# Performance work log

Measured on AMD Instinct MI355X. Metric: run time of the kernel, lower is better.

Reference implementation:

```python
import jax, jax.numpy as jnp
import numpy as np

N, D, K = 10000, 784, 16          # nodes, input feat dim, num_neighbors
E = N * (K - 1)                   # edges
H = 128                           # hidden width in all MLPs
SIZES = [784, 128, 2]             # node_sizes


def setup_inputs() -> dict:
    key = jax.random.key(0)
    ks = jax.random.split(key, 24)
    w = lambda k, shape: jax.random.normal(k, shape, jnp.float32) * 0.02
    inp = {
        "x": jax.random.normal(ks[0], (N, D), jnp.float32),
        "edge_attr": jax.random.uniform(ks[1], (E, 1), jnp.float32),
        "idxs": jax.random.randint(ks[2], (N, K - 1), 0, N, dtype=jnp.int32),
    }
    # Layer 1: in=784, msg_size=784, out=128
    inp["l1_msg_w1"] = w(ks[3], (D + 1, H));      inp["l1_msg_b1"] = jnp.zeros((H,), jnp.float32)
    inp["l1_msg_w2"] = w(ks[4], (H, D));          inp["l1_msg_b2"] = jnp.zeros((D,), jnp.float32)
    inp["l1_node_w1"] = w(ks[5], (D + D, H));     inp["l1_node_b1"] = jnp.zeros((H,), jnp.float32)
    inp["l1_node_w2"] = w(ks[6], (H, 128));       inp["l1_node_b2"] = jnp.zeros((128,), jnp.float32)
    # Layer 2: in=128, msg_size=128, out=2
    inp["l2_msg_w1"] = w(ks[7], (128 + 1, H));    inp["l2_msg_b1"] = jnp.zeros((H,), jnp.float32)
    inp["l2_msg_w2"] = w(ks[8], (H, 128));        inp["l2_msg_b2"] = jnp.zeros((128,), jnp.float32)
    inp["l2_node_w1"] = w(ks[9], (128 + 128, H)); inp["l2_node_b1"] = jnp.zeros((H,), jnp.float32)
    inp["l2_node_w2"] = w(ks[10], (H, 2));        inp["l2_node_b2"] = jnp.zeros((2,), jnp.float32)
    return inp


def _mlp(x, w1, b1, w2, b2):
    return jax.nn.relu(x @ w1 + b1) @ w2 + b2


def _node_layer(x, src, edge_attr,
                mw1, mb1, mw2, mb2, nw1, nb1, nw2, nb2):
    # message over edges: cat(x[src], edge_attr) -> MLP   [E, msg_size]
    msg = _mlp(jnp.concatenate([x[src], edge_attr], axis=1), mw1, mb1, mw2, mb2)
    # scatter_mean by src index (faithful to the original, which uses index=src)
    sums = jax.ops.segment_sum(msg, src, num_segments=N)
    cnt = jax.ops.segment_sum(jnp.ones((src.shape[0], 1), msg.dtype), src, num_segments=N)
    agg = jnp.where(cnt > 0, sums / jnp.maximum(cnt, 1.0), 0.0)
    # node update: cat(x, agg_msg) -> MLP
    return _mlp(jnp.concatenate([x, agg], axis=1), nw1, nb1, nw2, nb2)


def reference(x, edge_attr, idxs,
              l1_msg_w1, l1_msg_b1, l1_msg_w2, l1_msg_b2,
              l1_node_w1, l1_node_b1, l1_node_w2, l1_node_b2,
              l2_msg_w1, l2_msg_b1, l2_msg_w2, l2_msg_b2,
              l2_node_w1, l2_node_b1, l2_node_w2, l2_node_b2):
    src = idxs.reshape(-1)  # [E]; dst is unused by the original message computation
    h = _node_layer(x, src, edge_attr,
                    l1_msg_w1, l1_msg_b1, l1_msg_w2, l1_msg_b2,
                    l1_node_w1, l1_node_b1, l1_node_w2, l1_node_b2)
    proj = _node_layer(h, src, edge_attr,
                       l2_msg_w1, l2_msg_b1, l2_msg_w2, l2_msg_b2,
                       l2_node_w1, l2_node_b1, l2_node_w2, l2_node_b2)  # [N, 2]
    # vectorized per-neighbor squared distances (replaces the nested python loop)
    neigh = proj[idxs]                                   # [N, K-1, 2]
    d = jnp.sum((proj[:, None, :] - neigh) ** 2, axis=-1)  # [N, K-1]
    return d.reshape(-1, 1)                              # [N*(K-1), 1]
```

## Files before the change

### kernel.cpp

```cpp
#include <hip/hip_runtime.h>

#define N_NODES 10000
#define E_EDGES 150000
#define KNB     15
#define FILL_BLOCKS 587
#define GEMM_BLOCKS 628

__global__ void count_kernel(const int* __restrict__ idxs, int* __restrict__ cnt, int e) {
    int i = blockIdx.x * blockDim.x + threadIdx.x;
    if (i < e) atomicAdd(&cnt[idxs[i]], 1);
}

__device__ __forceinline__
void gemm_tile2(const float* __restrict__ A, int K,
                const float* __restrict__ Blo, const float* __restrict__ Bhi, int ldB,
                float* __restrict__ C, int ldC, int M,
                int rowBlk, int colBlk) {
    __shared__ float As2[16][34];
    __shared__ float Bs2[16][64];
    int tid = threadIdx.x;
    int tn  = tid & 15, tm = tid >> 4;
    int arow = tid >> 3, acB = (tid & 7) << 1;
    int brow = tid >> 4, bcol = (tid & 15) << 2;
    int rowBase = rowBlk * 32, colBase = colBlk * 64;

    bool half = (Bhi != nullptr) && (colBase >= 128);
    const float* B = half ? Bhi : Blo;
    int bj = colBase - (half ? 128 : 0) + bcol;

    float2 av; float4 bv;
    auto loadA = [&](int k0, float2& dst) {
        int gr = rowBase + arow;
        if (gr < M) dst = *(const float2*)(A + (size_t)gr * K + k0 + acB);
        else { dst.x = dst.y = 0.f; }
    };
    auto loadB = [&](int k0, float4& dst) {
        dst = *(const float4*)(B + (size_t)(k0 + brow) * ldB + bj);
    };
    loadA(0, av); loadB(0, bv);

    float acc[2][4] = {};
    for (int k0 = 0; k0 < K; k0 += 16) {
        __syncthreads();
        As2[acB + 0][arow] = av.x; As2[acB + 1][arow] = av.y;
        *(float4*)&Bs2[brow][bcol] = bv;
        __syncthreads();
        if (k0 + 16 < K) { loadA(k0 + 16, av); loadB(k0 + 16, bv); }
#pragma unroll
        for (int k = 0; k < 16; ++k) {
            float4 b = *(const float4*)&Bs2[k][tn << 2];
            float2 a = *(const float2*)&As2[k][tm << 1];
            acc[0][0] = fmaf(a.x, b.x, acc[0][0]); acc[0][1] = fmaf(a.x, b.y, acc[0][1]);
            acc[0][2] = fmaf(a.x, b.z, acc[0][2]); acc[0][3] = fmaf(a.x, b.w, acc[0][3]);
            acc[1][0] = fmaf(a.y, b.x, acc[1][0]); acc[1][1] = fmaf(a.y, b.y, acc[1][1]);
            acc[1][2] = fmaf(a.y, b.z, acc[1][2]); acc[1][3] = fmaf(a.y, b.w, acc[1][3]);
        }
    }
#pragma unroll
    for (int i = 0; i < 2; ++i) {
        int row = rowBase + tm * 2 + i;
        if (row >= M) continue;
#pragma unroll
        for (int j = 0; j < 4; ++j)
            C[(size_t)row * ldC + colBase + (tn << 2) + j] = acc[i][j];
    }
}

__global__ __launch_bounds__(256)
void scanfold_kernel(const float* __restrict__ mw2, const float* __restrict__ mb2,
                     const float* __restrict__ nw1, const float* __restrict__ nb2,
                     const float* __restrict__ nw2,
                     const float* __restrict__ m2w1, const float* __restrict__ m2b1,
                     const float* __restrict__ m2w2, const float* __restrict__ m2b2,
                     const float* __restrict__ n2w1, const float* __restrict__ n2b1,
                     float* __restrict__ M1, float* __restrict__ M2,
                     float* __restrict__ WH,
                     float* __restrict__ v1, float* __restrict__ v2,
                     float* __restrict__ bu2, float* __restrict__ bx2,
                     const int* __restrict__ cnt, int* __restrict__ eoff,
                     float* __restrict__ maskv, int* __restrict__ fillc) {
    int b = blockIdx.x;
    if (b == 0) {
        __shared__ int ssum[256];
        int tid = threadIdx.x;
        const int CH = 40;
        int base = tid * CH;
        int v[CH]; int s = 0;
#pragma unroll
        for (int q = 0; q < CH; ++q) {
            int i = base + q;
            v[q] = (i < N_NODES) ? cnt[i] : 0;
            s += v[q];
        }
        ssum[tid] = s;
        __syncthreads();
        for (int off = 1; off < 256; off <<= 1) {
            int t = (tid >= off) ? ssum[tid - off] : 0;
            __syncthreads();
            ssum[tid] += t;
            __syncthreads();
        }
        int ex = ssum[tid] - s;
#pragma unroll
        for (int q = 0; q < CH; ++q) {
            int i = base + q;
            if (i < N_NODES) {
                eoff[i]  = ex;
                maskv[i] = (v[q] > 0) ? 1.f : 0.f;
                fillc[i] = 0;
                ex += v[q];
            }
        }
        return;
    }
    b -= 1;
    if (b < 8) {
        gemm_tile2(mw2, 784, nw1 + 784 * 128, nullptr, 128, M1, 128, 128, b >> 1, b & 1);
    } else if (b < 16) {
        int t = b - 8;
        gemm_tile2(m2w2, 128, n2w1 + 128 * 128, nullptr, 128, M2, 128, 128, t >> 1, t & 1);
    } else if (b < 32) {
        int t = b - 16;
        gemm_tile2(nw2, 128, m2w1, n2w1, 128, WH, 256, 128, t >> 2, t & 3);
    } else {
        __shared__ float red[256];
        int t  = (b - 32) >> 1;
        int j  = ((b - 32) & 1) * 64 + (threadIdx.x & 63);
        int kq = threadIdx.x >> 6;
        const float* bvec; const float* Bv; const float* add; float* out; int Kv;
        if (t == 0)      { bvec = mb2;  Bv = nw1 + 784 * 128;  add = nullptr; out = v1;  Kv = 784; }
        else if (t == 1) { bvec = m2b2; Bv = n2w1 + 128 * 128; add = nullptr; out = v2;  Kv = 128; }
        else if (t == 2) { bvec = nb2;  Bv = m2w1;             add = m2b1;    out = bu2; Kv = 128; }
        else             { bvec = nb2;  Bv = n2w1;             add = n2b1;    out = bx2; Kv = 128; }
        float acc = 0.f;
        for (int k = kq; k < Kv; k += 4) acc = fmaf(bvec[k], Bv[k * 128 + j], acc);
        red[threadIdx.x] = acc;
        __syncthreads();
        if (threadIdx.x < 64) {
            float tot = red[threadIdx.x] + red[threadIdx.x + 64] +
                        red[threadIdx.x + 128] + red[threadIdx.x + 192];
            out[j] = tot + (add ? add[j] : 0.f);
        }
    }
}

__device__ __forceinline__
void gemm784_tile(const float* __restrict__ A,
                  const float* __restrict__ B0, const float* __restrict__ B1,
                  const float* __restrict__ biasLo, const float* __restrict__ biasHi,
                  const float* __restrict__ vhi, const float* __restrict__ rowmask,
                  float* __restrict__ C, int M, int gb) {
    __shared__ float As[16][68];
    __shared__ float Bs[16][64];
    int rb = gb >> 2, cb = gb & 3;
    int tid = threadIdx.x;
    int tm = tid >> 4, tn = tid & 15;
    int arow = tid >> 2, ac4 = (tid & 3) << 2;
    int brow = tid >> 4, bc4 = (tid & 15) << 2;
    int rowBase = rb * 64, colBase = cb * 64;
    bool hi = colBase >= 128;
    const float* B    = hi ? B1 : B0;
    const float* bias = hi ? biasHi : biasLo;
    int bj = ((cb & 1) << 6) + bc4;

    int gr = rowBase + arow; if (gr > M - 1) gr = M - 1;
    const float* Ap = A + (size_t)gr * 784;

    float4 av, bv;
    av = *(const float4*)(Ap + ac4);
    bv = *(const float4*)(B + (size_t)brow * 128 + bj);

    float acc[4][4] = {};
    for (int k0 = 0; k0 < 784; k0 += 16) {
        __syncthreads();
        As[ac4 + 0][arow] = av.x;
        As[ac4 + 1][arow] = av.y;
        As[ac4 + 2][arow] = av.z;
        As[ac4 + 3][arow] = av.w;
        *(float4*)&Bs[brow][bc4] = bv;
        __syncthreads();
        if (k0 + 16 < 784) {
            av = *(const float4*)(Ap + k0 + 16 + ac4);
            bv = *(const float4*)(B + (size_t)(k0 + 16 + brow) * 128 + bj);
        }
#pragma unroll
        for (int k = 0; k < 16; ++k) {
            float4 a = *(const float4*)&As[k][tm << 2];
            float4 b = *(const float4*)&Bs[k][tn << 2];
            acc[0][0] = fmaf(a.x, b.x, acc[0][0]); acc[0][1] = fmaf(a.x, b.y, acc[0][1]);
            acc[0][2] = fmaf(a.x, b.z, acc[0][2]); acc[0][3] = fmaf(a.x, b.w, acc[0][3]);
            acc[1][0] = fmaf(a.y, b.x, acc[1][0]); acc[1][1] = fmaf(a.y, b.y, acc[1][1]);
            acc[1][2] = fmaf(a.y, b.z, acc[1][2]); acc[1][3] = fmaf(a.y, b.w, acc[1][3]);
            acc[2][0] = fmaf(a.z, b.x, acc[2][0]); acc[2][1] = fmaf(a.z, b.y, acc[2][1]);
            acc[2][2] = fmaf(a.z, b.z, acc[2][2]); acc[2][3] = fmaf(a.z, b.w, acc[2][3]);
            acc[3][0] = fmaf(a.w, b.x, acc[3][0]); acc[3][1] = fmaf(a.w, b.y, acc[3][1]);
            acc[3][2] = fmaf(a.w, b.z, acc[3][2]); acc[3][3] = fmaf(a.w, b.w, acc[3][3]);
        }
    }

#pragma unroll
    for (int i = 0; i < 4; ++i) {
        int row = rowBase + (tm << 2) + i;
        if (row >= M) continue;
        float rm = hi ? rowmask[row] : 0.f;
#pragma unroll
        for (int j = 0; j < 4; ++j) {
            int gcol = colBase + (tn << 2) + j;
            int cj   = gcol & 127;
            float v = acc[i][j] + bias[cj];
            if (hi) v = fmaf(rm, vhi[cj], v);
            C[(size_t)row * 256 + gcol] = v;
        }
    }
}

__global__ __launch_bounds__(256)
void fillgemm_kernel(const int* __restrict__ idxs, const float* __restrict__ ea,
                     const int* __restrict__ eoff, int* __restrict__ fillc,
                     float* __restrict__ eas,
                     const float* __restrict__ A,
                     const float* __restrict__ B0, const float* __restrict__ B1,
                     const float* __restrict__ biasLo, const float* __restrict__ biasHi,
                     const float* __restrict__ vhi, const float* __restrict__ rowmask,
                     float* __restrict__ C, int M) {
    int gb = blockIdx.x;
    if (gb < FILL_BLOCKS) {
        int i = gb * 256 + threadIdx.x;
        if (i < E_EDGES) {
            int s = idxs[i];
            int p = atomicAdd(&fillc[s], 1);
            eas[eoff[s] + p] = ea[i];
        }
        return;
    }
    gemm784_tile(A, B0, B1, biasLo, biasHi, vhi, rowmask, C, M, gb - FILL_BLOCKS);
}

__global__ __launch_bounds__(256)
void fused_mid_kernel(const float* __restrict__ UX, const float* __restrict__ wlast,
                      const float* __restrict__ eas, const int* __restrict__ eoff,
                      const int* __restrict__ cnt,
                      const float* __restrict__ Mmat, const float* __restrict__ WH,
                      const float* __restrict__ bu2, const float* __restrict__ bx2,
                      const float* __restrict__ v2,
                      float* __restrict__ UX2, int M) {
    __shared__ float mhT[128][36];
    __shared__ float ts[32][132];
    __shared__ float Bs[16][264];
    __shared__ float ebuf[1536];
    __shared__ float rmask[32];
    int rowBase = blockIdx.x * 32;
    int tid = threadIdx.x;

    {
        int d = tid & 127, sub = tid >> 7;
        float w = wlast[d];
        float uu[16], sum[16];
        int es[16], ec[16];
#pragma unroll
        for (int it = 0; it < 16; ++it) {
            int n  = rowBase + it * 2 + sub;
            int nc = (n < M) ? n : M - 1;
            ec[it] = cnt[nc];
            es[it] = eoff[nc];
            uu[it] = UX[(size_t)nc * 256 + d];
            sum[it] = 0.f;
            if (d == 0) rmask[it * 2 + sub] = (ec[it] > 0) ? 1.f : 0.f;
        }
        int ebase = eoff[rowBase];
        int eend  = (rowBase + 32 < M) ? eoff[rowBase + 32] : E_EDGES;
        for (int w0 = ebase; w0 < eend; w0 += 1536) {
            int wlen = min(1536, eend - w0);
            __syncthreads();
            for (int q = tid; q < wlen; q += 256) ebuf[q] = eas[w0 + q];
            __syncthreads();
#pragma unroll
            for (int it = 0; it < 16; ++it) {
                int lo = max(es[it], w0), hi = min(es[it] + ec[it], w0 + wlen);
                for (int e = lo; e < hi; ++e)
                    sum[it] += fmaxf(fmaf(ebuf[e - w0], w, uu[it]), 0.f);
            }
        }
#pragma unroll
        for (int it = 0; it < 16; ++it)
            mhT[d][it * 2 + sub] = (ec[it] > 0) ? sum[it] / (float)ec[it] : 0.f;
    }
    __syncthreads();

    {
        int tm = tid >> 5, tn = tid & 31;
        float acc[4][4] = {};
        for (int k0 = 0; k0 < 128; k0 += 16) {
#pragma unroll
            for (int t2 = 0; t2 < 2; ++t2) {
                int f2 = (tid << 1) | t2;
                int kr = f2 >> 5, c4 = (f2 & 31) << 2;
                *(float4*)&Bs[kr][c4] = *(const float4*)(Mmat + (size_t)(k0 + kr) * 128 + c4);
            }
            __syncthreads();
#pragma unroll
            for (int k = 0; k < 16; ++k) {
                float4 a = *(const float4*)&mhT[k0 + k][tm << 2];
                float4 b = *(const float4*)&Bs[k][tn << 2];
                acc[0][0] = fmaf(a.x, b.x, acc[0][0]); acc[0][1] = fmaf(a.x, b.y, acc[0][1]);
                acc[0][2] = fmaf(a.x, b.z, acc[0][2]); acc[0][3] = fmaf(a.x, b.w, acc[0][3]);
                acc[1][0] = fmaf(a.y, b.x, acc[1][0]); acc[1][1] = fmaf(a.y, b.y, acc[1][1]);
                acc[1][2] = fmaf(a.y, b.z, acc[1][2]); acc[1][3] = fmaf(a.y, b.w, acc[1][3]);
                acc[2][0] = fmaf(a.z, b.x, acc[2][0]); acc[2][1] = fmaf(a.z, b.y, acc[2][1]);
                acc[2][2] = fmaf(a.z, b.z, acc[2][2]); acc[2][3] = fmaf(a.z, b.w, acc[2][3]);
                acc[3][0] = fmaf(a.w, b.x, acc[3][0]); acc[3][1] = fmaf(a.w, b.y, acc[3][1]);
                acc[3][2] = fmaf(a.w, b.z, acc[3][2]); acc[3][3] = fmaf(a.w, b.w, acc[3][3]);
            }
            __syncthreads();
        }
#pragma unroll
        for (int i = 0; i < 4; ++i) {
            int row = rowBase + (tm << 2) + i;
            int rc  = (row < M) ? row : M - 1;
#pragma unroll
            for (int j = 0; j < 4; ++j) {
                int col = (tn << 2) + j;
                float v = acc[i][j] + UX[(size_t)rc * 256 + 128 + col];
                ts[(tm << 2) + i][col] = fmaxf(v, 0.f);
            }
        }
    }

    {
        int tm = tid >> 5, tn = tid & 31;
        float acc[4][8] = {};
        for (int k0 = 0; k0 < 128; k0 += 16) {
#pragma unroll
            for (int q = 0; q < 4; ++q) {
                int slot = (q << 8) + tid;
                int kr = slot >> 6, c4 = (slot & 63) << 2;
                *(float4*)&Bs[kr][c4] = *(const float4*)(WH + (size_t)(k0 + kr) * 256 + c4);
            }
            __syncthreads();
#pragma unroll
            for (int k = 0; k < 16; ++k) {
                float4 b0 = *(const float4*)&Bs[k][tn << 3];
                float4 b1 = *(const float4*)&Bs[k][(tn << 3) + 4];
                float br[8] = {b0.x, b0.y, b0.z, b0.w, b1.x, b1.y, b1.z, b1.w};
#pragma unroll
                for (int i = 0; i < 4; ++i) {
                    float a = ts[(tm << 2) + i][k0 + k];
#pragma unroll
                    for (int j = 0; j < 8; ++j)
                        acc[i][j] = fmaf(a, br[j], acc[i][j]);
                }
            }
            __syncthreads();
        }
        bool half = (tn >= 16);
        const float* bias = half ? bx2 : bu2;
#pragma unroll
        for (int i = 0; i < 4; ++i) {
            int row = rowBase + (tm << 2) + i;
            if (row >= M) continue;
            float rm = rmask[(tm << 2) + i];
            float4 o0, o1;
            float* po0 = (float*)&o0; float* po1 = (float*)&o1;
#pragma unroll
            for (int j = 0; j < 4; ++j) {
                int gcol0 = (tn << 3) + j, gcol1 = (tn << 3) + 4 + j;
                int cj0 = gcol0 & 127, cj1 = gcol1 & 127;
                float v0 = acc[i][j] + bias[cj0];
                float v1s = acc[i][4 + j] + bias[cj1];
                if (half) { v0 = fmaf(rm, v2[cj0], v0); v1s = fmaf(rm, v2[cj1], v1s); }
                po0[j] = v0; po1[j] = v1s;
            }
            float* orow = UX2 + (size_t)row * 256 + (tn << 3);
            *(float4*)(orow)     = o0;
            *(float4*)(orow + 4) = o1;
        }
    }
}

__global__ __launch_bounds__(256)
void fused_last_kernel(const float* __restrict__ UX2, const float* __restrict__ wlast,
                       const float* __restrict__ eas, const int* __restrict__ eoff,
                       const int* __restrict__ cnt,
                       const float* __restrict__ Mmat,
                       const float* __restrict__ w2, const float* __restrict__ b2,
                       float* __restrict__ proj, int M) {
    __shared__ float mhT[128][36];
    __shared__ float Bs[16][132];
    __shared__ float ebuf[1536];
    int rowBase = blockIdx.x * 32;
    int tid = threadIdx.x;

    {
        int d = tid & 127, sub = tid >> 7;
        float w = wlast[d];
        float uu[16], sum[16];
        int es[16], ec[16];
#pragma unroll
        for (int it = 0; it < 16; ++it) {
            int n  = rowBase + it * 2 + sub;
            int nc = (n < M) ? n : M - 1;
            ec[it] = cnt[nc];
            es[it] = eoff[nc];
            uu[it] = UX2[(size_t)nc * 256 + d];
            sum[it] = 0.f;
        }
        int ebase = eoff[rowBase];
        int eend  = (rowBase + 32 < M) ? eoff[rowBase + 32] : E_EDGES;
        for (int w0 = ebase; w0 < eend; w0 += 1536) {
            int wlen = min(1536, eend - w0);
            __syncthreads();
            for (int q = tid; q < wlen; q += 256) ebuf[q] = eas[w0 + q];
            __syncthreads();
#pragma unroll
            for (int it = 0; it < 16; ++it) {
                int lo = max(es[it], w0), hi = min(es[it] + ec[it], w0 + wlen);
                for (int e = lo; e < hi; ++e)
                    sum[it] += fmaxf(fmaf(ebuf[e - w0], w, uu[it]), 0.f);
            }
        }
#pragma unroll
        for (int it = 0; it < 16; ++it)
            mhT[d][it * 2 + sub] = (ec[it] > 0) ? sum[it] / (float)ec[it] : 0.f;
    }
    __syncthreads();

    int tm = tid >> 5, tn = tid & 31;
    float acc[4][4] = {};
    for (int k0 = 0; k0 < 128; k0 += 16) {
#pragma unroll
        for (int t2 = 0; t2 < 2; ++t2) {
            int f2 = (tid << 1) | t2;
            int kr = f2 >> 5, c4 = (f2 & 31) << 2;
            *(float4*)&Bs[kr][c4] = *(const float4*)(Mmat + (size_t)(k0 + kr) * 128 + c4);
        }
        __syncthreads();
#pragma unroll
        for (int k = 0; k < 16; ++k) {
            float4 a = *(const float4*)&mhT[k0 + k][tm << 2];
            float4 b = *(const float4*)&Bs[k][tn << 2];
            acc[0][0] = fmaf(a.x, b.x, acc[0][0]); acc[0][1] = fmaf(a.x, b.y, acc[0][1]);
            acc[0][2] = fmaf(a.x, b.z, acc[0][2]); acc[0][3] = fmaf(a.x, b.w, acc[0][3]);
            acc[1][0] = fmaf(a.y, b.x, acc[1][0]); acc[1][1] = fmaf(a.y, b.y, acc[1][1]);
            acc[1][2] = fmaf(a.y, b.z, acc[1][2]); acc[1][3] = fmaf(a.y, b.w, acc[1][3]);
            acc[2][0] = fmaf(a.z, b.x, acc[2][0]); acc[2][1] = fmaf(a.z, b.y, acc[2][1]);
            acc[2][2] = fmaf(a.z, b.z, acc[2][2]); acc[2][3] = fmaf(a.z, b.w, acc[2][3]);
            acc[3][0] = fmaf(a.w, b.x, acc[3][0]); acc[3][1] = fmaf(a.w, b.y, acc[3][1]);
            acc[3][2] = fmaf(a.w, b.z, acc[3][2]); acc[3][3] = fmaf(a.w, b.w, acc[3][3]);
        }
        __syncthreads();
    }

    float p0[4] = {}, p1[4] = {};
#pragma unroll
    for (int i = 0; i < 4; ++i) {
        int row = rowBase + (tm << 2) + i;
        int rc  = (row < M) ? row : M - 1;
#pragma unroll
        for (int j = 0; j < 4; ++j) {
            int col = (tn << 2) + j;
            float t = fmaxf(acc[i][j] + UX2[(size_t)rc * 256 + 128 + col], 0.f);
            p0[i] = fmaf(t, w2[col * 2],     p0[i]);
            p1[i] = fmaf(t, w2[col * 2 + 1], p1[i]);
        }
    }
#pragma unroll
    for (int i = 0; i < 4; ++i) {
        for (int off = 16; off > 0; off >>= 1) {
            p0[i] += __shfl_xor(p0[i], off, 64);
            p1[i] += __shfl_xor(p1[i], off, 64);
        }
    }
    if (tn == 0) {
#pragma unroll
        for (int i = 0; i < 4; ++i) {
            int row = rowBase + (tm << 2) + i;
            if (row < M) {
                proj[row * 2]     = p0[i] + b2[0];
                proj[row * 2 + 1] = p1[i] + b2[1];
            }
        }
    }
}

__global__ void dist_kernel(const float* __restrict__ proj, const int* __restrict__ idxs,
                            float* __restrict__ out, int e) {
    int i = blockIdx.x * blockDim.x + threadIdx.x;
    if (i >= e) return;
    int n = i / KNB;
    int m = idxs[i];
    float2 pn = *(const float2*)(proj + 2 * n);
    float2 pm = *(const float2*)(proj + 2 * m);
    float dx = pn.x - pm.x;
    float dy = pn.y - pm.y;
    out[i] = dx * dx + dy * dy;
}

extern "C" void kernel_launch(void* const* d_in, const int* in_sizes, int n_in,
                              void* d_out, int out_size, void* d_ws, size_t ws_size,
                              hipStream_t stream) {
    (void)in_sizes; (void)n_in; (void)out_size; (void)ws_size;
    const float* x    = (const float*)d_in[0];
    const float* eatt = (const float*)d_in[1];
    const int*   idxs = (const int*)d_in[2];
    const float* mw1  = (const float*)d_in[3];
    const float* mb1  = (const float*)d_in[4];
    const float* mw2  = (const float*)d_in[5];
    const float* mb2  = (const float*)d_in[6];
    const float* nw1  = (const float*)d_in[7];
    const float* nb1  = (const float*)d_in[8];
    const float* nw2  = (const float*)d_in[9];
    const float* nb2  = (const float*)d_in[10];
    const float* m2w1 = (const float*)d_in[11];
    const float* m2b1 = (const float*)d_in[12];
    const float* m2w2 = (const float*)d_in[13];
    const float* m2b2 = (const float*)d_in[14];
    const float* n2w1 = (const float*)d_in[15];
    const float* n2b1 = (const float*)d_in[16];
    const float* n2w2 = (const float*)d_in[17];
    const float* n2b2 = (const float*)d_in[18];
    float* out = (float*)d_out;

    float* fws   = (float*)d_ws;
    float* UX1   = fws;
    float* UX2   = fws + 2560000;
    float* proj  = fws + 5120000;
    float* maskv = fws + 5140000;
    float* eas   = fws + 5150016;
    float* M1    = fws + 5300016;
    float* M2    = fws + 5316400;
    float* WH    = fws + 5332784;
    float* v1    = fws + 5365552;
    float* v2    = fws + 5365680;
    float* bu2   = fws + 5365808;
    float* bx2   = fws + 5365936;
    int*   cnt   = (int*)(fws + 5366064);
    int*   fillc = cnt + N_NODES;
    int*   eoff  = fillc + N_NODES;

    hipMemsetAsync(cnt, 0, N_NODES * sizeof(int), stream);
    count_kernel<<<FILL_BLOCKS, 256, 0, stream>>>(idxs, cnt, E_EDGES);

    scanfold_kernel<<<41, 256, 0, stream>>>(mw2, mb2, nw1, nb2, nw2,
                                            m2w1, m2b1, m2w2, m2b2, n2w1, n2b1,
                                            M1, M2, WH, v1, v2, bu2, bx2,
                                            cnt, eoff, maskv, fillc);

    fillgemm_kernel<<<FILL_BLOCKS + GEMM_BLOCKS, 256, 0, stream>>>(
        idxs, eatt, eoff, fillc, eas,
        x, mw1, nw1, mb1, nb1, v1, maskv, UX1, N_NODES);

    fused_mid_kernel<<<313, 256, 0, stream>>>(UX1, mw1 + 784 * 128, eas, eoff, cnt,
                                              M1, WH, bu2, bx2, v2, UX2, N_NODES);

    fused_last_kernel<<<313, 256, 0, stream>>>(UX2, m2w1 + 128 * 128, eas, eoff, cnt,
                                               M2, n2w2, n2b2, proj, N_NODES);

    dist_kernel<<<FILL_BLOCKS, 256, 0, stream>>>(proj, idxs, out, E_EDGES);
}
```

Measured before the change: 302.8 us.

## Fuse layer-1 GEMM, both message phases and node MLPs into one per-row kernel

```diff
diff --git a/kernel.cpp b/kernel.cpp
--- a/kernel.cpp
+++ b/kernel.cpp
@@ -3,8 +3,7 @@
 #define N_NODES 10000
 #define E_EDGES 150000
 #define KNB     15
-#define FILL_BLOCKS 587
-#define GEMM_BLOCKS 628
+#define EBLOCKS 587
 
 __global__ void count_kernel(const int* __restrict__ idxs, int* __restrict__ cnt, int e) {
     int i = blockIdx.x * blockDim.x + threadIdx.x;
@@ -144,198 +143,186 @@
     }
 }
 
-__device__ __forceinline__
-void gemm784_tile(const float* __restrict__ A,
-                  const float* __restrict__ B0, const float* __restrict__ B1,
-                  const float* __restrict__ biasLo, const float* __restrict__ biasHi,
-                  const float* __restrict__ vhi, const float* __restrict__ rowmask,
-                  float* __restrict__ C, int M, int gb) {
-    __shared__ float As[16][68];
-    __shared__ float Bs[16][64];
-    int rb = gb >> 2, cb = gb & 3;
+__global__ void fill_kernel(const int* __restrict__ idxs, const float* __restrict__ ea,
+                            const int* __restrict__ eoff, int* __restrict__ fillc,
+                            float* __restrict__ eas, int e) {
+    int i = blockIdx.x * blockDim.x + threadIdx.x;
+    if (i < e) {
+        int s = idxs[i];
+        int p = atomicAdd(&fillc[s], 1);
+        eas[eoff[s] + p] = ea[i];
+    }
+}
+
+__global__ __launch_bounds__(256)
+void meganode_kernel(const float* __restrict__ x,
+                     const float* __restrict__ mw1, const float* __restrict__ nw1,
+                     const float* __restrict__ mb1, const float* __restrict__ nb1,
+                     const float* __restrict__ v1, const float* __restrict__ maskv,
+                     const float* __restrict__ w1last,
+                     const float* __restrict__ eas, const int* __restrict__ eoff,
+                     const int* __restrict__ cnt,
+                     const float* __restrict__ M1, const float* __restrict__ WH,
+                     const float* __restrict__ bu2, const float* __restrict__ bx2,
+                     const float* __restrict__ v2,
+                     const float* __restrict__ w2last,
+                     const float* __restrict__ M2,
+                     const float* __restrict__ pw, const float* __restrict__ pb,
+                     float* __restrict__ UX1, float* __restrict__ UX2,
+                     float* __restrict__ proj) {
+    __shared__ float As[16][20];
+    __shared__ float Bs[16][264];
+    __shared__ float mhT[128][18];
+    __shared__ float ts[16][132];
+    __shared__ float ebuf[1024];
+    int rowBase = blockIdx.x * 16;
     int tid = threadIdx.x;
-    int tm = tid >> 4, tn = tid & 15;
-    int arow = tid >> 2, ac4 = (tid & 3) << 2;
-    int brow = tid >> 4, bc4 = (tid & 15) << 2;
-    int rowBase = rb * 64, colBase = cb * 64;
-    bool hi = colBase >= 128;
-    const float* B    = hi ? B1 : B0;
-    const float* bias = hi ? biasHi : biasLo;
-    int bj = ((cb & 1) << 6) + bc4;
-
-    int gr = rowBase + arow; if (gr > M - 1) gr = M - 1;
-    const float* Ap = A + (size_t)gr * 784;
-
-    float4 av, bv;
-    av = *(const float4*)(Ap + ac4);
-    bv = *(const float4*)(B + (size_t)brow * 128 + bj);
-
-    float acc[4][4] = {};
-    for (int k0 = 0; k0 < 784; k0 += 16) {
-        __syncthreads();
-        As[ac4 + 0][arow] = av.x;
-        As[ac4 + 1][arow] = av.y;
-        As[ac4 + 2][arow] = av.z;
-        As[ac4 + 3][arow] = av.w;
-        *(float4*)&Bs[brow][bc4] = bv;
-        __syncthreads();
-        if (k0 + 16 < 784) {
-            av = *(const float4*)(Ap + k0 + 16 + ac4);
-            bv = *(const float4*)(B + (size_t)(k0 + 16 + brow) * 128 + bj);
-        }
-#pragma unroll
-        for (int k = 0; k < 16; ++k) {
-            float4 a = *(const float4*)&As[k][tm << 2];
-            float4 b = *(const float4*)&Bs[k][tn << 2];
-            acc[0][0] = fmaf(a.x, b.x, acc[0][0]); acc[0][1] = fmaf(a.x, b.y, acc[0][1]);
-            acc[0][2] = fmaf(a.x, b.z, acc[0][2]); acc[0][3] = fmaf(a.x, b.w, acc[0][3]);
-            acc[1][0] = fmaf(a.y, b.x, acc[1][0]); acc[1][1] = fmaf(a.y, b.y, acc[1][1]);
-            acc[1][2] = fmaf(a.y, b.z, acc[1][2]); acc[1][3] = fmaf(a.y, b.w, acc[1][3]);
-            acc[2][0] = fmaf(a.z, b.x, acc[2][0]); acc[2][1] = fmaf(a.z, b.y, acc[2][1]);
-            acc[2][2] = fmaf(a.z, b.z, acc[2][2]); acc[2][3] = fmaf(a.z, b.w, acc[2][3]);
-            acc[3][0] = fmaf(a.w, b.x, acc[3][0]); acc[3][1] = fmaf(a.w, b.y, acc[3][1]);
-            acc[3][2] = fmaf(a.w, b.z, acc[3][2]); acc[3][3] = fmaf(a.w, b.w, acc[3][3]);
-        }
-    }
-
-#pragma unroll
-    for (int i = 0; i < 4; ++i) {
-        int row = rowBase + (tm << 2) + i;
-        if (row >= M) continue;
-        float rm = hi ? rowmask[row] : 0.f;
-#pragma unroll
-        for (int j = 0; j < 4; ++j) {
-            int gcol = colBase + (tn << 2) + j;
-            int cj   = gcol & 127;
-            float v = acc[i][j] + bias[cj];
-            if (hi) v = fmaf(rm, vhi[cj], v);
-            C[(size_t)row * 256 + gcol] = v;
-        }
-    }
-}
-
-__global__ __launch_bounds__(256)
-void fillgemm_kernel(const int* __restrict__ idxs, const float* __restrict__ ea,
-                     const int* __restrict__ eoff, int* __restrict__ fillc,
-                     float* __restrict__ eas,
-                     const float* __restrict__ A,
-                     const float* __restrict__ B0, const float* __restrict__ B1,
-                     const float* __restrict__ biasLo, const float* __restrict__ biasHi,
-                     const float* __restrict__ vhi, const float* __restrict__ rowmask,
-                     float* __restrict__ C, int M) {
-    int gb = blockIdx.x;
-    if (gb < FILL_BLOCKS) {
-        int i = gb * 256 + threadIdx.x;
-        if (i < E_EDGES) {
-            int s = idxs[i];
-            int p = atomicAdd(&fillc[s], 1);
-            eas[eoff[s] + p] = ea[i];
-        }
-        return;
-    }
-    gemm784_tile(A, B0, B1, biasLo, biasHi, vhi, rowmask, C, M, gb - FILL_BLOCKS);
-}
-
-__global__ __launch_bounds__(256)
-void fused_mid_kernel(const float* __restrict__ UX, const float* __restrict__ wlast,
-                      const float* __restrict__ eas, const int* __restrict__ eoff,
-                      const int* __restrict__ cnt,
-                      const float* __restrict__ Mmat, const float* __restrict__ WH,
-                      const float* __restrict__ bu2, const float* __restrict__ bx2,
-                      const float* __restrict__ v2,
-                      float* __restrict__ UX2, int M) {
-    __shared__ float mhT[128][36];
-    __shared__ float ts[32][132];
-    __shared__ float Bs[16][264];
-    __shared__ float ebuf[1536];
-    __shared__ float rmask[32];
-    int rowBase = blockIdx.x * 32;
-    int tid = threadIdx.x;
+    int tm2 = tid >> 5;
+    int tn  = tid & 31;
 
     {
+        int bkr = tid >> 4, bc4 = (tid & 15) << 2;
+        float4 aA; float4 bB[4];
+        auto gload = [&](int k0) {
+            if (tid < 64) {
+                int row = tid >> 2, kq = (tid & 3) << 2;
+                aA = *(const float4*)(x + (size_t)(rowBase + row) * 784 + k0 + kq);
+            }
+#pragma unroll
+            for (int p = 0; p < 4; ++p) {
+                int col = bc4 + p * 64;
+                const float* Bp = (col < 128)
+                    ? (mw1 + (size_t)(k0 + bkr) * 128 + col)
+                    : (nw1 + (size_t)(k0 + bkr) * 128 + (col - 128));
+                bB[p] = *(const float4*)Bp;
+            }
+        };
+        auto sstore = [&]() {
+            if (tid < 64) {
+                int row = tid >> 2, kq = (tid & 3) << 2;
+                As[kq + 0][row] = aA.x; As[kq + 1][row] = aA.y;
+                As[kq + 2][row] = aA.z; As[kq + 3][row] = aA.w;
+            }
+#pragma unroll
+            for (int p = 0; p < 4; ++p)
+                *(float4*)&Bs[bkr][bc4 + p * 64] = bB[p];
+        };
+        gload(0);
+        float acc[2][8] = {};
+        for (int k0 = 0; k0 < 784; k0 += 16) {
+            __syncthreads();
+            sstore();
+            __syncthreads();
+            if (k0 + 16 < 784) gload(k0 + 16);
+#pragma unroll
+            for (int k = 0; k < 16; ++k) {
+                float2 a  = *(const float2*)&As[k][tm2 << 1];
+                float4 b0 = *(const float4*)&Bs[k][tn << 3];
+                float4 b1 = *(const float4*)&Bs[k][(tn << 3) + 4];
+                float br[8] = {b0.x, b0.y, b0.z, b0.w, b1.x, b1.y, b1.z, b1.w};
+#pragma unroll
+                for (int j = 0; j < 8; ++j) {
+                    acc[0][j] = fmaf(a.x, br[j], acc[0][j]);
+                    acc[1][j] = fmaf(a.y, br[j], acc[1][j]);
+                }
+            }
+        }
+        bool hi = tn >= 16;
+        const float* bias = hi ? nb1 : mb1;
+#pragma unroll
+        for (int i = 0; i < 2; ++i) {
+            int row = rowBase + (tm2 << 1) + i;
+            float rm = hi ? maskv[row] : 0.f;
+            float4 o0, o1; float* po0 = (float*)&o0; float* po1 = (float*)&o1;
+#pragma unroll
+            for (int j = 0; j < 4; ++j) {
+                int cj0 = ((tn << 3) + j) & 127, cj1 = ((tn << 3) + 4 + j) & 127;
+                float q0 = acc[i][j]     + bias[cj0];
+                float q1 = acc[i][4 + j] + bias[cj1];
+                if (hi) { q0 = fmaf(rm, v1[cj0], q0); q1 = fmaf(rm, v1[cj1], q1); }
+                po0[j] = q0; po1[j] = q1;
+            }
+            float* orow = UX1 + (size_t)row * 256 + (tn << 3);
+            *(float4*)orow       = o0;
+            *(float4*)(orow + 4) = o1;
+        }
+    }
+    __syncthreads();
+
+    auto msg_phase = [&](const float* __restrict__ U, const float* __restrict__ wl) {
         int d = tid & 127, sub = tid >> 7;
-        float w = wlast[d];
-        float uu[16], sum[16];
-        int es[16], ec[16];
-#pragma unroll
-        for (int it = 0; it < 16; ++it) {
+        float w = wl[d];
+        float uu[8], sum[8];
+        int es[8], ec[8];
+#pragma unroll
+        for (int it = 0; it < 8; ++it) {
             int n  = rowBase + it * 2 + sub;
-            int nc = (n < M) ? n : M - 1;
-            ec[it] = cnt[nc];
-            es[it] = eoff[nc];
-            uu[it] = UX[(size_t)nc * 256 + d];
+            ec[it] = cnt[n];
+            es[it] = eoff[n];
+            uu[it] = U[(size_t)n * 256 + d];
             sum[it] = 0.f;
-            if (d == 0) rmask[it * 2 + sub] = (ec[it] > 0) ? 1.f : 0.f;
         }
         int ebase = eoff[rowBase];
-        int eend  = (rowBase + 32 < M) ? eoff[rowBase + 32] : E_EDGES;
-        for (int w0 = ebase; w0 < eend; w0 += 1536) {
-            int wlen = min(1536, eend - w0);
+        int eend  = (rowBase + 16 < N_NODES) ? eoff[rowBase + 16] : E_EDGES;
+        for (int w0 = ebase; w0 < eend; w0 += 1024) {
+            int wlen = min(1024, eend - w0);
             __syncthreads();
             for (int q = tid; q < wlen; q += 256) ebuf[q] = eas[w0 + q];
             __syncthreads();
 #pragma unroll
-            for (int it = 0; it < 16; ++it) {
-                int lo = max(es[it], w0), hi = min(es[it] + ec[it], w0 + wlen);
-                for (int e = lo; e < hi; ++e)
+            for (int it = 0; it < 8; ++it) {
+                int lo = max(es[it], w0), hiE = min(es[it] + ec[it], w0 + wlen);
+                for (int e = lo; e < hiE; ++e)
                     sum[it] += fmaxf(fmaf(ebuf[e - w0], w, uu[it]), 0.f);
             }
         }
 #pragma unroll
-        for (int it = 0; it < 16; ++it)
+        for (int it = 0; it < 8; ++it)
             mhT[d][it * 2 + sub] = (ec[it] > 0) ? sum[it] / (float)ec[it] : 0.f;
-    }
+    };
+
+    msg_phase(UX1, w1last);
     __syncthreads();
 
     {
-        int tm = tid >> 5, tn = tid & 31;
-        float acc[4][4] = {};
+        float acc[2][4] = {};
         for (int k0 = 0; k0 < 128; k0 += 16) {
-#pragma unroll
-            for (int t2 = 0; t2 < 2; ++t2) {
-                int f2 = (tid << 1) | t2;
-                int kr = f2 >> 5, c4 = (f2 & 31) << 2;
-                *(float4*)&Bs[kr][c4] = *(const float4*)(Mmat + (size_t)(k0 + kr) * 128 + c4);
-            }
+            int kr = tid >> 4, c8 = (tid & 15) << 3;
+            *(float4*)&Bs[kr][c8]     = *(const float4*)(M1 + (size_t)(k0 + kr) * 128 + c8);
+            *(float4*)&Bs[kr][c8 + 4] = *(const float4*)(M1 + (size_t)(k0 + kr) * 128 + c8 + 4);
             __syncthreads();
 #pragma unroll
             for (int k = 0; k < 16; ++k) {
-                float4 a = *(const float4*)&mhT[k0 + k][tm << 2];
+                float2 a = *(const float2*)&mhT[k0 + k][tm2 << 1];
                 float4 b = *(const float4*)&Bs[k][tn << 2];
                 acc[0][0] = fmaf(a.x, b.x, acc[0][0]); acc[0][1] = fmaf(a.x, b.y, acc[0][1]);
                 acc[0][2] = fmaf(a.x, b.z, acc[0][2]); acc[0][3] = fmaf(a.x, b.w, acc[0][3]);
                 acc[1][0] = fmaf(a.y, b.x, acc[1][0]); acc[1][1] = fmaf(a.y, b.y, acc[1][1]);
                 acc[1][2] = fmaf(a.y, b.z, acc[1][2]); acc[1][3] = fmaf(a.y, b.w, acc[1][3]);
-                acc[2][0] = fmaf(a.z, b.x, acc[2][0]); acc[2][1] = fmaf(a.z, b.y, acc[2][1]);
-                acc[2][2] = fmaf(a.z, b.z, acc[2][2]); acc[2][3] = fmaf(a.z, b.w, acc[2][3]);
-                acc[3][0] = fmaf(a.w, b.x, acc[3][0]); acc[3][1] = fmaf(a.w, b.y, acc[3][1]);
-                acc[3][2] = fmaf(a.w, b.z, acc[3][2]); acc[3][3] = fmaf(a.w, b.w, acc[3][3]);
-            }
-            __syncthreads();
-        }
-#pragma unroll
-        for (int i = 0; i < 4; ++i) {
-            int row = rowBase + (tm << 2) + i;
-            int rc  = (row < M) ? row : M - 1;
-#pragma unroll
-            for (int j = 0; j < 4; ++j) {
-                int col = (tn << 2) + j;
-                float v = acc[i][j] + UX[(size_t)rc * 256 + 128 + col];
-                ts[(tm << 2) + i][col] = fmaxf(v, 0.f);
-            }
+            }
+            __syncthreads();
+        }
+#pragma unroll
+        for (int i = 0; i < 2; ++i) {
+            int row = rowBase + (tm2 << 1) + i;
+            float4 xn = *(const float4*)(UX1 + (size_t)row * 256 + 128 + (tn << 2));
+            float4 o;
+            o.x = fmaxf(acc[i][0] + xn.x, 0.f);
+            o.y = fmaxf(acc[i][1] + xn.y, 0.f);
+            o.z = fmaxf(acc[i][2] + xn.z, 0.f);
+            o.w = fmaxf(acc[i][3] + xn.w, 0.f);
+            *(float4*)&ts[(tm2 << 1) + i][tn << 2] = o;
         }
     }
 
     {
-        int tm = tid >> 5, tn = tid & 31;
-        float acc[4][8] = {};
+        float acc[2][8] = {};
         for (int k0 = 0; k0 < 128; k0 += 16) {
-#pragma unroll
-            for (int q = 0; q < 4; ++q) {
-                int slot = (q << 8) + tid;
-                int kr = slot >> 6, c4 = (slot & 63) << 2;
-                *(float4*)&Bs[kr][c4] = *(const float4*)(WH + (size_t)(k0 + kr) * 256 + c4);
-            }
+            int kr = tid >> 4, c4 = (tid & 15) << 2;
+#pragma unroll
+            for (int p = 0; p < 4; ++p)
+                *(float4*)&Bs[kr][c4 + p * 64] =
+                    *(const float4*)(WH + (size_t)(k0 + kr) * 256 + c4 + p * 64);
             __syncthreads();
 #pragma unroll
             for (int k = 0; k < 16; ++k) {
@@ -343,8 +330,8 @@
                 float4 b1 = *(const float4*)&Bs[k][(tn << 3) + 4];
                 float br[8] = {b0.x, b0.y, b0.z, b0.w, b1.x, b1.y, b1.z, b1.w};
 #pragma unroll
-                for (int i = 0; i < 4; ++i) {
-                    float a = ts[(tm << 2) + i][k0 + k];
+                for (int i = 0; i < 2; ++i) {
+                    float a = ts[(tm2 << 1) + i][k0 + k];
 #pragma unroll
                     for (int j = 0; j < 8; ++j)
                         acc[i][j] = fmaf(a, br[j], acc[i][j]);
@@ -352,131 +339,73 @@
             }
             __syncthreads();
         }
-        bool half = (tn >= 16);
-        const float* bias = half ? bx2 : bu2;
-#pragma unroll
-        for (int i = 0; i < 4; ++i) {
-            int row = rowBase + (tm << 2) + i;
-            if (row >= M) continue;
-            float rm = rmask[(tm << 2) + i];
-            float4 o0, o1;
-            float* po0 = (float*)&o0; float* po1 = (float*)&o1;
+        bool hi = tn >= 16;
+        const float* bias = hi ? bx2 : bu2;
+#pragma unroll
+        for (int i = 0; i < 2; ++i) {
+            int row = rowBase + (tm2 << 1) + i;
+            float rm = maskv[row];
+            float4 o0, o1; float* po0 = (float*)&o0; float* po1 = (float*)&o1;
 #pragma unroll
             for (int j = 0; j < 4; ++j) {
-                int gcol0 = (tn << 3) + j, gcol1 = (tn << 3) + 4 + j;
-                int cj0 = gcol0 & 127, cj1 = gcol1 & 127;
-                float v0 = acc[i][j] + bias[cj0];
-                float v1s = acc[i][4 + j] + bias[cj1];
-                if (half) { v0 = fmaf(rm, v2[cj0], v0); v1s = fmaf(rm, v2[cj1], v1s); }
-                po0[j] = v0; po1[j] = v1s;
+                int cj0 = ((tn << 3) + j) & 127, cj1 = ((tn << 3) + 4 + j) & 127;
+                float q0 = acc[i][j]     + bias[cj0];
+                float q1 = acc[i][4 + j] + bias[cj1];
+                if (hi) { q0 = fmaf(rm, v2[cj0], q0); q1 = fmaf(rm, v2[cj1], q1); }
+                po0[j] = q0; po1[j] = q1;
             }
             float* orow = UX2 + (size_t)row * 256 + (tn << 3);
-            *(float4*)(orow)     = o0;
+            *(float4*)orow       = o0;
             *(float4*)(orow + 4) = o1;
         }
     }
-}
-
-__global__ __launch_bounds__(256)
-void fused_last_kernel(const float* __restrict__ UX2, const float* __restrict__ wlast,
-                       const float* __restrict__ eas, const int* __restrict__ eoff,
-                       const int* __restrict__ cnt,
-                       const float* __restrict__ Mmat,
-                       const float* __restrict__ w2, const float* __restrict__ b2,
-                       float* __restrict__ proj, int M) {
-    __shared__ float mhT[128][36];
-    __shared__ float Bs[16][132];
-    __shared__ float ebuf[1536];
-    int rowBase = blockIdx.x * 32;
-    int tid = threadIdx.x;
+    __syncthreads();
+
+    msg_phase(UX2, w2last);
 
     {
-        int d = tid & 127, sub = tid >> 7;
-        float w = wlast[d];
-        float uu[16], sum[16];
-        int es[16], ec[16];
-#pragma unroll
-        for (int it = 0; it < 16; ++it) {
-            int n  = rowBase + it * 2 + sub;
-            int nc = (n < M) ? n : M - 1;
-            ec[it] = cnt[nc];
-            es[it] = eoff[nc];
-            uu[it] = UX2[(size_t)nc * 256 + d];
-            sum[it] = 0.f;
-        }
-        int ebase = eoff[rowBase];
-        int eend  = (rowBase + 32 < M) ? eoff[rowBase + 32] : E_EDGES;
-        for (int w0 = ebase; w0 < eend; w0 += 1536) {
-            int wlen = min(1536, eend - w0);
-            __syncthreads();
-            for (int q = tid; q < wlen; q += 256) ebuf[q] = eas[w0 + q];
-            __syncthreads();
-#pragma unroll
-            for (int it = 0; it < 16; ++it) {
-                int lo = max(es[it], w0), hi = min(es[it] + ec[it], w0 + wlen);
-                for (int e = lo; e < hi; ++e)
-                    sum[it] += fmaxf(fmaf(ebuf[e - w0], w, uu[it]), 0.f);
-            }
-        }
-#pragma unroll
-        for (int it = 0; it < 16; ++it)
-            mhT[d][it * 2 + sub] = (ec[it] > 0) ? sum[it] / (float)ec[it] : 0.f;
-    }
-    __syncthreads();
-
-    int tm = tid >> 5, tn = tid & 31;
-    float acc[4][4] = {};
-    for (int k0 = 0; k0 < 128; k0 += 16) {
-#pragma unroll
-        for (int t2 = 0; t2 < 2; ++t2) {
-            int f2 = (tid << 1) | t2;
-            int kr = f2 >> 5, c4 = (f2 & 31) << 2;
-            *(float4*)&Bs[kr][c4] = *(const float4*)(Mmat + (size_t)(k0 + kr) * 128 + c4);
-        }
-        __syncthreads();
-#pragma unroll
-        for (int k = 0; k < 16; ++k) {
-            float4 a = *(const float4*)&mhT[k0 + k][tm << 2];
-            float4 b = *(const float4*)&Bs[k][tn << 2];
-            acc[0][0] = fmaf(a.x, b.x, acc[0][0]); acc[0][1] = fmaf(a.x, b.y, acc[0][1]);
-            acc[0][2] = fmaf(a.x, b.z, acc[0][2]); acc[0][3] = fmaf(a.x, b.w, acc[0][3]);
-            acc[1][0] = fmaf(a.y, b.x, acc[1][0]); acc[1][1] = fmaf(a.y, b.y, acc[1][1]);
-            acc[1][2] = fmaf(a.y, b.z, acc[1][2]); acc[1][3] = fmaf(a.y, b.w, acc[1][3]);
-            acc[2][0] = fmaf(a.z, b.x, acc[2][0]); acc[2][1] = fmaf(a.z, b.y, acc[2][1]);
-            acc[2][2] = fmaf(a.z, b.z, acc[2][2]); acc[2][3] = fmaf(a.z, b.w, acc[2][3]);
-            acc[3][0] = fmaf(a.w, b.x, acc[3][0]); acc[3][1] = fmaf(a.w, b.y, acc[3][1]);
-            acc[3][2] = fmaf(a.w, b.z, acc[3][2]); acc[3][3] = fmaf(a.w, b.w, acc[3][3]);
-        }
-        __syncthreads();
-    }
-
-    float p0[4] = {}, p1[4] = {};
-#pragma unroll
-    for (int i = 0; i < 4; ++i) {
-        int row = rowBase + (tm << 2) + i;
-        int rc  = (row < M) ? row : M - 1;
-#pragma unroll
-        for (int j = 0; j < 4; ++j) {
-            int col = (tn << 2) + j;
-            float t = fmaxf(acc[i][j] + UX2[(size_t)rc * 256 + 128 + col], 0.f);
-            p0[i] = fmaf(t, w2[col * 2],     p0[i]);
-            p1[i] = fmaf(t, w2[col * 2 + 1], p1[i]);
-        }
-    }
-#pragma unroll
-    for (int i = 0; i < 4; ++i) {
+        float acc[2][4] = {};
+        for (int k0 = 0; k0 < 128; k0 += 16) {
+            int kr = tid >> 4, c8 = (tid & 15) << 3;
+            *(float4*)&Bs[kr][c8]     = *(const float4*)(M2 + (size_t)(k0 + kr) * 128 + c8);
+            *(float4*)&Bs[kr][c8 + 4] = *(const float4*)(M2 + (size_t)(k0 + kr) * 128 + c8 + 4);
+            __syncthreads();
+#pragma unroll
+            for (int k = 0; k < 16; ++k) {
+                float2 a = *(const float2*)&mhT[k0 + k][tm2 << 1];
+                float4 b = *(const float4*)&Bs[k][tn << 2];
+                acc[0][0] = fmaf(a.x, b.x, acc[0][0]); acc[0][1] = fmaf(a.x, b.y, acc[0][1]);
+                acc[0][2] = fmaf(a.x, b.z, acc[0][2]); acc[0][3] = fmaf(a.x, b.w, acc[0][3]);
+                acc[1][0] = fmaf(a.y, b.x, acc[1][0]); acc[1][1] = fmaf(a.y, b.y, acc[1][1]);
+                acc[1][2] = fmaf(a.y, b.z, acc[1][2]); acc[1][3] = fmaf(a.y, b.w, acc[1][3]);
+            }
+            __syncthreads();
+        }
+        float pp0[2], pp1[2];
+#pragma unroll
+        for (int i = 0; i < 2; ++i) {
+            int row = rowBase + (tm2 << 1) + i;
+            float4 xn = *(const float4*)(UX2 + (size_t)row * 256 + 128 + (tn << 2));
+            float t0 = fmaxf(acc[i][0] + xn.x, 0.f);
+            float t1 = fmaxf(acc[i][1] + xn.y, 0.f);
+            float t2 = fmaxf(acc[i][2] + xn.z, 0.f);
+            float t3 = fmaxf(acc[i][3] + xn.w, 0.f);
+            int c = tn << 2;
+            pp0[i] = fmaf(t3, pw[2*(c+3)],   fmaf(t2, pw[2*(c+2)],   fmaf(t1, pw[2*(c+1)],   t0 * pw[2*c])));
+            pp1[i] = fmaf(t3, pw[2*(c+3)+1], fmaf(t2, pw[2*(c+2)+1], fmaf(t1, pw[2*(c+1)+1], t0 * pw[2*c+1])));
+        }
         for (int off = 16; off > 0; off >>= 1) {
-            p0[i] += __shfl_xor(p0[i], off, 64);
-            p1[i] += __shfl_xor(p1[i], off, 64);
-        }
-    }
-    if (tn == 0) {
-#pragma unroll
-        for (int i = 0; i < 4; ++i) {
-            int row = rowBase + (tm << 2) + i;
-            if (row < M) {
-                proj[row * 2]     = p0[i] + b2[0];
-                proj[row * 2 + 1] = p1[i] + b2[1];
+            pp0[0] += __shfl_xor(pp0[0], off, 64);
+            pp0[1] += __shfl_xor(pp0[1], off, 64);
+            pp1[0] += __shfl_xor(pp1[0], off, 64);
+            pp1[1] += __shfl_xor(pp1[1], off, 64);
+        }
+        if (tn == 0) {
+#pragma unroll
+            for (int i = 0; i < 2; ++i) {
+                int row = rowBase + (tm2 << 1) + i;
+                proj[2 * row]     = pp0[i] + pb[0];
+                proj[2 * row + 1] = pp1[i] + pb[1];
             }
         }
     }
@@ -538,22 +467,22 @@
     int*   eoff  = fillc + N_NODES;
 
     hipMemsetAsync(cnt, 0, N_NODES * sizeof(int), stream);
-    count_kernel<<<FILL_BLOCKS, 256, 0, stream>>>(idxs, cnt, E_EDGES);
+    count_kernel<<<EBLOCKS, 256, 0, stream>>>(idxs, cnt, E_EDGES);
 
     scanfold_kernel<<<41, 256, 0, stream>>>(mw2, mb2, nw1, nb2, nw2,
                                             m2w1, m2b1, m2w2, m2b2, n2w1, n2b1,
                                             M1, M2, WH, v1, v2, bu2, bx2,
                                             cnt, eoff, maskv, fillc);
 
-    fillgemm_kernel<<<FILL_BLOCKS + GEMM_BLOCKS, 256, 0, stream>>>(
-        idxs, eatt, eoff, fillc, eas,
-        x, mw1, nw1, mb1, nb1, v1, maskv, UX1, N_NODES);
-
-    fused_mid_kernel<<<313, 256, 0, stream>>>(UX1, mw1 + 784 * 128, eas, eoff, cnt,
-                                              M1, WH, bu2, bx2, v2, UX2, N_NODES);
-
-    fused_last_kernel<<<313, 256, 0, stream>>>(UX2, m2w1 + 128 * 128, eas, eoff, cnt,
-                                               M2, n2w2, n2b2, proj, N_NODES);
-
-    dist_kernel<<<FILL_BLOCKS, 256, 0, stream>>>(proj, idxs, out, E_EDGES);
-}
+    fill_kernel<<<EBLOCKS, 256, 0, stream>>>(idxs, eatt, eoff, fillc, eas, E_EDGES);
+
+    meganode_kernel<<<625, 256, 0, stream>>>(x, mw1, nw1, mb1, nb1, v1, maskv,
+                                             mw1 + 784 * 128,
+                                             eas, eoff, cnt,
+                                             M1, WH, bu2, bx2, v2,
+                                             m2w1 + 128 * 128,
+                                             M2, n2w2, n2b2,
+                                             UX1, UX2, proj);
+
+    dist_kernel<<<EBLOCKS, 256, 0, stream>>>(proj, idxs, out, E_EDGES);
+}
```

Measured after the change: 453.3 us. 1.5x slower.
